# Optimization experiments

Measured on AMD Instinct MI355X. Metric: run time of the kernel, lower is better.

Reference implementation:

```python
import jax, jax.numpy as jnp
import numpy as np

N, C, E, B, NPG, MAX_LEN, H, EF = 16384, 512, 524288, 64, 256, 512, 8, 16
EPS = 1e-5

def layernorm(x, g, b):
    m = jnp.mean(x, axis=-1, keepdims=True)
    v = jnp.mean(jnp.square(x - m), axis=-1, keepdims=True)
    return (x - m) / jnp.sqrt(v + EPS) * g + b

def setup_inputs() -> dict:
    key = jax.random.key(0)
    ks = list(jax.random.split(key, 32))
    x = jax.random.normal(ks[0], (N, C), dtype=jnp.float32)
    edge_attr = jax.random.normal(ks[1], (E, EF), dtype=jnp.float32)
    # edges within each graph of NPG nodes
    src = jax.random.randint(ks[2], (E,), 0, N)
    dst = (src // NPG) * NPG + jax.random.randint(ks[3], (E,), 0, NPG)
    edge_index = jnp.stack([src, dst]).astype(jnp.int64)
    batch = jnp.repeat(jnp.arange(B), NPG).astype(jnp.int64)  # sorted graph ids
    s = 0.03
    p = lambda k, shp: jax.random.normal(k, shp, dtype=jnp.float32) * s
    return dict(
        x=x, edge_attr=edge_attr,
        gcn_w=p(ks[4], (C, C)), gcn_b=jnp.zeros((C,)),
        ep_w=p(ks[5], (EF, C)), ep_b=jnp.zeros((C,)),
        gate_w=p(ks[6], (2 * C, C)), gate_b=jnp.zeros((C,)),
        n1_g=jnp.ones((C,)), n1_b=jnp.zeros((C,)),
        in_w=p(ks[7], (C, 3 * C)), in_b=jnp.zeros((3 * C,)),
        out_w=p(ks[8], (C, C)), out_b=jnp.zeros((C,)),
        tn_g=jnp.ones((C,)), tn_b=jnp.zeros((C,)),
        m_w1=p(ks[9], (C, 2 * C)), m_b1=jnp.zeros((2 * C,)),
        m_w2=p(ks[10], (2 * C, C)), m_b2=jnp.zeros((C,)),
        fn_g=jnp.ones((C,)), fn_b=jnp.zeros((C,)),
        edge_index=edge_index, batch=batch,
    )

def reference(x, edge_attr, gcn_w, gcn_b, ep_w, ep_b, gate_w, gate_b,
              n1_g, n1_b, in_w, in_b, out_w, out_b, tn_g, tn_b,
              m_w1, m_b1, m_w2, m_b2, fn_g, fn_b, edge_index, batch):
    src, dst = edge_index[0], edge_index[1]
    # --- CoGNN: weighted GCN conv (self-loops, sym norm) ---
    ew = jax.lax.stop_gradient(jnp.sqrt(jnp.sum(edge_attr * edge_attr, axis=-1)))
    loop = jnp.arange(N)
    src2 = jnp.concatenate([src, loop]); dst2 = jnp.concatenate([dst, loop])
    ew2 = jnp.concatenate([ew, jnp.ones((N,), ew.dtype)])
    deg = jax.ops.segment_sum(ew2, dst2, num_segments=N)
    dinv = jnp.where(deg > 0, jax.lax.rsqrt(jnp.maximum(deg, 1e-12)), 0.0)
    norm = dinv[src2] * ew2 * dinv[dst2]
    xw = x @ gcn_w
    x_conv = jax.ops.segment_sum(norm[:, None] * xw[src2], dst2, num_segments=N) + gcn_b
    # edge_proj -> scatter_add at source nodes (dropout = identity in eval)
    ef = jax.nn.relu(edge_attr @ ep_w + ep_b)
    ef = jax.ops.segment_sum(ef, src, num_segments=N)
    gate = jax.nn.sigmoid(jnp.concatenate([x_conv, ef], axis=-1) @ gate_w + gate_b)
    x1 = gate * x_conv + (1.0 - gate) * ef
    x1 = jax.nn.relu(layernorm(x1, n1_g, n1_b))
    x = x1 + x  # identity residual (in_channels == hidden_channels)
    # --- to_dense_batch ---
    counts = jax.ops.segment_sum(jnp.ones((N,), jnp.int32), batch, num_segments=B)
    starts = jnp.cumsum(counts) - counts
    pos = jnp.arange(N) - starts[batch]
    xd = jnp.zeros((B, MAX_LEN, C), x.dtype).at[batch, pos].set(x)
    maskd = jnp.zeros((B, MAX_LEN), bool).at[batch, pos].set(True)
    # --- MHA (batch_first, key_padding_mask = ~mask) ---
    Dh = C // H
    qkv = xd @ in_w + in_b
    q, k, v = jnp.split(qkv, 3, axis=-1)
    q = q.reshape(B, MAX_LEN, H, Dh); k = k.reshape(B, MAX_LEN, H, Dh); v = v.reshape(B, MAX_LEN, H, Dh)
    scores = jnp.einsum('blhd,bmhd->bhlm', q, k) / jnp.sqrt(jnp.asarray(Dh, x.dtype))
    scores = jnp.where(maskd[:, None, None, :], scores, -1e9)
    attn = jax.nn.softmax(scores, axis=-1)
    o = jnp.einsum('bhlm,bmhd->blhd', attn, v).reshape(B, MAX_LEN, C)
    o = o @ out_w + out_b
    x_global = o[batch, pos]  # undo dense batching: x_global[mask]
    x = layernorm(x + x_global, tn_g, tn_b)
    # --- MLP ---
    x = x + (jax.nn.silu(x @ m_w1 + m_b1) @ m_w2 + m_b2)
    return layernorm(x, fn_g, fn_b)
```

## Files before the change

### kernel.cpp

```cpp
#include <hip/hip_runtime.h>

#define NN 16384
#define CC 512
#define EE 524288
#define BB 64
#define HH 8
#define EFD 16
#define GEMAXE 10240

typedef __bf16 bf16_t;
typedef __bf16 bf16x4 __attribute__((ext_vector_type(4)));
typedef __bf16 bf16x8 __attribute__((ext_vector_type(8)));
typedef float f32x4v __attribute__((ext_vector_type(4)));

__device__ __forceinline__ float2 ldb2(const bf16_t* p) {
  unsigned w = *(const unsigned*)p;
  return make_float2(__uint_as_float(w << 16), __uint_as_float(w & 0xFFFF0000u));
}

__device__ __forceinline__ int2 xcd_swizzle() {
  int nwg = gridDim.x * gridDim.y;
  int bid = blockIdx.y * gridDim.x + blockIdx.x;
  int wg = (bid & 7) * (nwg >> 3) + (bid >> 3);
  return make_int2(wg % gridDim.x, wg / gridDim.x);
}


__global__ void init_kernel(int* ghist, int* nid_src, bf16_t* eacsr) {
  int i = threadIdx.x;
  if (i < 64) ghist[i] = 0;
  if (i < 32) nid_src[EE + i] = -1;
  ((int*)(eacsr + (size_t)EE * 16))[i] = 0;
}

__global__ __launch_bounds__(256) void edge_pass1(const int* __restrict__ dst,
                                                  int* ghist) {
  __shared__ int h[64];
  int tid = threadIdx.x;
  if (tid < 64) h[tid] = 0;
  __syncthreads();
  int e = blockIdx.x * 256 + tid;
  atomicAdd(&h[dst[e] >> 8], 1);
  __syncthreads();
  if (tid < 64 && h[tid]) atomicAdd(&ghist[tid], h[tid]);
}

__global__ void gexscan_kernel(const int* __restrict__ ghist, int* __restrict__ gstart,
                               int* __restrict__ gcur) {
  if (threadIdx.x == 0) {
    int s = 0;
    for (int g = 0; g < 64; ++g) { gstart[g] = s; gcur[g] = s; s += ghist[g]; }
    gstart[64] = s;
  }
}

__global__ __launch_bounds__(256) void graph_scatter_kernel(
    const int* __restrict__ src, const int* __restrict__ dst,
    const float* __restrict__ ea, int* gcur, int2* __restrict__ grec,
    float* __restrict__ ewg) {
  __shared__ int h[64], base[64], h2[64];
  int tid = threadIdx.x;
  if (tid < 64) { h[tid] = 0; h2[tid] = 0; }
  __syncthreads();
  int e0 = blockIdx.x * 2048;
  int gloc[8];
#pragma unroll
  for (int k = 0; k < 8; ++k) {
    gloc[k] = dst[e0 + k * 256 + tid] >> 8;
    atomicAdd(&h[gloc[k]], 1);
  }
  __syncthreads();
  if (tid < 64) base[tid] = h[tid] ? atomicAdd(&gcur[tid], h[tid]) : 0;
  __syncthreads();
#pragma unroll
  for (int k = 0; k < 8; ++k) {
    int e = e0 + k * 256 + tid;
    int g = gloc[k];
    int p = atomicAdd(&h2[g], 1);
    int pos = base[g] + p;
    int ls = src[e] & 255;
    int ld = dst[e] & 255;
    grec[pos] = make_int2(e | (ls << 19), ld);
    const float4* pa = (const float4*)(ea + (size_t)e * EFD);
    float s = 0.f;
#pragma unroll
    for (int q = 0; q < 4; ++q) {
      float4 v = pa[q];
      s += v.x * v.x + v.y * v.y + v.z * v.z + v.w * v.w;
    }
    ewg[pos] = sqrtf(s);
  }
}

__global__ __launch_bounds__(1024) void graph_sort2_kernel(
    const int2* __restrict__ grec, const float* __restrict__ ewg,
    const int* __restrict__ gstart, int* __restrict__ elist_src,
    int* __restrict__ nid_src, int* __restrict__ start_src,
    float2* __restrict__ dstrec, int* __restrict__ start_dst,
    float* __restrict__ dinv) {
  __shared__ int lbuf[GEMAXE];
  __shared__ unsigned short sl[GEMAXE];
  __shared__ float ewl[GEMAXE];
  __shared__ int h[256], hx[256], h2[256];
  __shared__ float fdinv[256];
  const int g = blockIdx.x & 63;
  const int tid = threadIdx.x;
  const int gs = gstart[g];
  const int cnt = gstart[g + 1] - gs;
  if (tid < 256) { h[tid] = 0; h2[tid] = 0; }
  __syncthreads();
  if (blockIdx.x < 64) {
    for (int i = tid; i < cnt; i += 1024) {
      int2 r = grec[gs + i];
      int ld = r.y;
      sl[i] = (unsigned short)(((r.x >> 19) & 255) | (ld << 8));
      ewl[i] = ewg[gs + i];
      atomicAdd(&h[ld], 1);
    }
    __syncthreads();
    int myc = (tid < 256) ? h[tid] : 0;
    for (int off = 1; off < 256; off <<= 1) {
      int v = (tid < 256 && tid >= off) ? h[tid - off] : 0;
      __syncthreads();
      if (tid < 256) h[tid] += v;
      __syncthreads();
    }
    if (tid < 256) {
      hx[tid] = h[tid] - myc;
      start_dst[g * 256 + tid] = gs + hx[tid];
    }
    if (g == 63 && tid == 0) start_dst[NN] = EE;
    __syncthreads();
    for (int i = tid; i < cnt; i += 1024) {
      int ld = sl[i] >> 8;
      int p = hx[ld] + atomicAdd(&h2[ld], 1);
      lbuf[p] = i;
    }
    __syncthreads();
    if (tid < 256) {
      float dg = 1.0f;
      int s0 = hx[tid], e0 = s0 + myc;
      for (int i = s0; i < e0; ++i) dg += ewl[lbuf[i]];
      float dv = rsqrtf(fmaxf(dg, 1e-12f));
      fdinv[tid] = dv;
      dinv[g * 256 + tid] = dv;
    }
    __syncthreads();
    for (int p = tid; p < cnt; p += 1024) {
      int i = lbuf[p];
      int ls = sl[i] & 255;
      int ld = sl[i] >> 8;
      dstrec[gs + p] =
          make_float2(fdinv[ls] * ewl[i] * fdinv[ld], __int_as_float(ls));
    }
  } else {
    int* wb = (int*)ewl;
    for (int i = tid; i < cnt; i += 1024) {
      int w = grec[gs + i].x;
      wb[i] = w;
      atomicAdd(&h[w >> 19], 1);
    }
    __syncthreads();
    int myc = (tid < 256) ? h[tid] : 0;
    for (int off = 1; off < 256; off <<= 1) {
      int v = (tid < 256 && tid >= off) ? h[tid - off] : 0;
      __syncthreads();
      if (tid < 256) h[tid] += v;
      __syncthreads();
    }
    if (tid < 256) {
      hx[tid] = h[tid] - myc;
      start_src[g * 256 + tid] = gs + hx[tid];
    }
    if (g == 63 && tid == 0) start_src[NN] = EE;
    __syncthreads();
    for (int i = tid; i < cnt; i += 1024) {
      int w = wb[i];
      int ls = w >> 19;
      int p = hx[ls] + atomicAdd(&h2[ls], 1);
      lbuf[p] = w;
    }
    __syncthreads();
    for (int p = tid; p < cnt; p += 1024) {
      int w = lbuf[p];
      elist_src[gs + p] = w & 0x7FFFF;
      nid_src[gs + p] = g * 256 + (w >> 19);
    }
  }
}

__global__ void ea_gather_kernel(const float* __restrict__ ea,
                                 const int* __restrict__ elist,
                                 bf16_t* __restrict__ eacsr) {
  int idx = blockIdx.x * 256 + threadIdx.x;
  if (idx >= EE * 2) return;
  int pos = idx >> 1, half = idx & 1;
  int e = elist[pos];
  const f32x4v* p = (const f32x4v*)(ea + (size_t)e * EFD + half * 8);
  f32x4v u0 = p[0], u1 = p[1];
  bf16x8 f;
#pragma unroll
  for (int r = 0; r < 4; ++r) {
    f[r] = (bf16_t)u0[r];
    f[4 + r] = (bf16_t)u1[r];
  }
  *(bf16x8*)(eacsr + (size_t)pos * 16 + half * 8) = f;
}

__global__ __launch_bounds__(256) void an_build_kernel(
    const float2* __restrict__ dstrec, const int* __restrict__ start_dst,
    const float* __restrict__ dinv, bf16_t* __restrict__ An) {
  __shared__ float AnS[128][256];
  const int g = blockIdx.x >> 1, h = blockIdx.x & 1;
  const int tid = threadIdx.x;
  float4* az = (float4*)&AnS[0][0];
  for (int i = tid; i < 128 * 256 / 4; i += 256)
    az[i] = make_float4(0.f, 0.f, 0.f, 0.f);
  __syncthreads();
  const int nbase = g * 256 + h * 128;
  if (tid < 128) {
    int node = nbase + tid;
    int st = start_dst[node], en = start_dst[node + 1];
    float* row = AnS[tid];
    for (int p = st; p < en; ++p) {
      float2 r = dstrec[p];
      row[__float_as_int(r.y)] += r.x;
    }
    float dv = dinv[node];
    row[h * 128 + tid] += dv * dv;
  }
  __syncthreads();
  bf16_t* out = An + (size_t)nbase * 256;
  const float* s0 = &AnS[0][0];
  for (int i = tid; i < 128 * 256 / 8; i += 256) {
    bf16x8 v;
#pragma unroll
    for (int r = 0; r < 8; ++r) v[r] = (bf16_t)s0[i * 8 + r];
    *(bf16x8*)(out + i * 8) = v;
  }
}


__global__ void cvt_bf16_kernel(const float* __restrict__ in, bf16_t* __restrict__ out,
                                int n4) {
  int i = blockIdx.x * 256 + threadIdx.x;
  if (i >= n4) return;
  float4 v = ((const float4*)in)[i];
  bf16x4 o;
  o[0] = (bf16_t)v.x; o[1] = (bf16_t)v.y; o[2] = (bf16_t)v.z; o[3] = (bf16_t)v.w;
  ((bf16x4*)out)[i] = o;
}

__global__ __launch_bounds__(256) void wt_kernel(const float* __restrict__ W,
                                                 bf16_t* __restrict__ Wt, int K, int N) {
  __shared__ float tile[32][33];
  int bx = blockIdx.x * 32;
  int by = blockIdx.y * 32;
  int tx = threadIdx.x & 31, ty = threadIdx.x >> 5;
#pragma unroll
  for (int i = 0; i < 32; i += 8)
    tile[ty + i][tx] = W[(size_t)(by + ty + i) * N + bx + tx];
  __syncthreads();
#pragma unroll
  for (int i = 0; i < 32; i += 8)
    Wt[(size_t)(bx + ty + i) * K + by + tx] = (bf16_t)tile[tx][ty + i];
}

__global__ __launch_bounds__(512) void ef_mfma_kernel(
    const bf16_t* __restrict__ eacsr, const float* __restrict__ ep_w,
    const float* __restrict__ ep_b, const int* __restrict__ nid,
    const int* __restrict__ start, bf16_t* __restrict__ efb) {
  const int tid = threadIdx.x;
  const int lane = tid & 63;
  const int wv = tid >> 6;
  const int l15 = lane & 15;
  const int g = lane >> 4;
  const int n0 = blockIdx.x * 16;
  const int cbase = wv * 64;

  bf16x8 wfr[4];
#pragma unroll
  for (int t = 0; t < 4; ++t) {
    bf16x8 f = {};
    int c = cbase + t * 16 + l15;
    if (g < 2) {
#pragma unroll
      for (int j = 0; j < 8; ++j) f[j] = (bf16_t)ep_w[(g * 8 + j) * CC + c];
    } else if (g == 2) {
      f[0] = (bf16_t)ep_b[c];
    }
    wfr[t] = f;
  }

  const int st = start[n0];
  const int en = start[n0 + 16];
  const int tgt = n0 + l15;

  f32x4v eacc[4] = {};

  for (int cb = st; cb < en; cb += 32) {
    bf16x8 af[2];
#pragma unroll
    for (int mE = 0; mE < 2; ++mE) {
      bf16x8 f = {};
      if (g < 2) {
        f = *(const bf16x8*)(eacsr + (size_t)(cb + mE * 16 + l15) * 16 + g * 8);
      } else if (g == 2) {
        f[0] = (bf16_t)1.0f;
      }
      af[mE] = f;
    }
    int4 idlo = *(const int4*)(nid + cb + g * 4);
    int4 idhi = *(const int4*)(nid + cb + 16 + g * 4);
    bf16x8 sf;
    sf[0] = (idlo.x == tgt) ? (bf16_t)1.0f : (bf16_t)0.0f;
    sf[1] = (idlo.y == tgt) ? (bf16_t)1.0f : (bf16_t)0.0f;
    sf[2] = (idlo.z == tgt) ? (bf16_t)1.0f : (bf16_t)0.0f;
    sf[3] = (idlo.w == tgt) ? (bf16_t)1.0f : (bf16_t)0.0f;
    sf[4] = (idhi.x == tgt) ? (bf16_t)1.0f : (bf16_t)0.0f;
    sf[5] = (idhi.y == tgt) ? (bf16_t)1.0f : (bf16_t)0.0f;
    sf[6] = (idhi.z == tgt) ? (bf16_t)1.0f : (bf16_t)0.0f;
    sf[7] = (idhi.w == tgt) ? (bf16_t)1.0f : (bf16_t)0.0f;
#pragma unroll
    for (int t = 0; t < 4; ++t) {
      f32x4v s0 = {}, s1 = {};
      s0 = __builtin_amdgcn_mfma_f32_16x16x32_bf16(af[0], wfr[t], s0, 0, 0, 0);
      s1 = __builtin_amdgcn_mfma_f32_16x16x32_bf16(af[1], wfr[t], s1, 0, 0, 0);
      union { bf16x8 v; bf16x4 h[2]; } pf;
#pragma unroll
      for (int r = 0; r < 4; ++r) {
        pf.h[0][r] = (bf16_t)fmaxf(s0[r], 0.f);
        pf.h[1][r] = (bf16_t)fmaxf(s1[r], 0.f);
      }
      eacc[t] = __builtin_amdgcn_mfma_f32_16x16x32_bf16(sf, pf.v, eacc[t], 0, 0, 0);
    }
  }
#pragma unroll
  for (int t = 0; t < 4; ++t) {
    int c = cbase + t * 16 + l15;
#pragma unroll
    for (int r = 0; r < 4; ++r) {
      int node = n0 + g * 4 + r;
      efb[(size_t)node * (2 * CC) + CC + c] = (bf16_t)eacc[t][r];
    }
  }
}

__device__ __forceinline__ void gl_lds16(const bf16_t* g, bf16_t* l) {
  __builtin_amdgcn_global_load_lds(
      (const __attribute__((address_space(1))) void*)g,
      (__attribute__((address_space(3))) void*)l, 16, 0, 0);
}

template <int ACT, int OUT>
__global__ __launch_bounds__(256) void gemm_bf16_kernel(
    const bf16_t* __restrict__ A, const bf16_t* __restrict__ Bt,
    const float* __restrict__ bias, void* __restrict__ Cout, int M, int N, int K) {
  __shared__ __align__(16) bf16_t Al[128 * 64];
  __shared__ __align__(16) bf16_t Bl[128 * 64];
  const int tid = threadIdx.x;
  const int lane = tid & 63;
  const int wave = tid >> 6;
  int2 sw = xcd_swizzle();
  const int row0 = sw.y * 128;
  const int col0 = sw.x * 128;
  const int wm = (wave >> 1) * 64;
  const int wn = (wave & 1) * 64;
  f32x4v acc[4][4] = {};
  const int srow = wave * 8 + (lane >> 3);
  const int sslot = (lane & 7) ^ (lane >> 3);
  const bf16_t* aBase = A + (size_t)(row0 + srow) * K + sslot * 8;
  const bf16_t* bBase = Bt + (size_t)(col0 + srow) * K + sslot * 8;
  const int fr = lane & 15;
  const int g = lane >> 4;
  const int f7 = fr & 7;
  for (int k0 = 0; k0 < K; k0 += 64) {
#pragma unroll
    for (int i = 0; i < 4; ++i)
      gl_lds16(aBase + (size_t)(i * 32) * K + k0, Al + i * 2048 + wave * 512);
#pragma unroll
    for (int i = 0; i < 4; ++i)
      gl_lds16(bBase + (size_t)(i * 32) * K + k0, Bl + i * 2048 + wave * 512);
    __syncthreads();
#pragma unroll
    for (int s = 0; s < 2; ++s) {
      const int sl = ((s * 4 + g) ^ f7) * 8;
      bf16x8 af[4], bfv[4];
#pragma unroll
      for (int m = 0; m < 4; ++m)
        af[m] = *(const bf16x8*)(Al + (wm + m * 16 + fr) * 64 + sl);
#pragma unroll
      for (int n = 0; n < 4; ++n)
        bfv[n] = *(const bf16x8*)(Bl + (wn + n * 16 + fr) * 64 + sl);
#pragma unroll
      for (int m = 0; m < 4; ++m)
#pragma unroll
        for (int n = 0; n < 4; ++n)
          acc[m][n] = __builtin_amdgcn_mfma_f32_16x16x32_bf16(af[m], bfv[n],
                                                              acc[m][n], 0, 0, 0);
    }
    __syncthreads();
  }
  const int fq = (lane >> 4) * 4;
#pragma unroll
  for (int m = 0; m < 4; ++m) {
    int grb = row0 + wm + m * 16 + fq;
#pragma unroll
    for (int n = 0; n < 4; ++n) {
      int gc = col0 + wn + n * 16 + fr;
      float bv = bias ? bias[gc] : 0.f;
#pragma unroll
      for (int r = 0; r < 4; ++r) {
        float v = acc[m][n][r] + bv;
        if (ACT == 1) v = v / (1.f + __expf(-v));
        if (OUT == 0)
          ((float*)Cout)[(size_t)(grb + r) * N + gc] = v;
        else
          ((bf16_t*)Cout)[(size_t)(grb + r) * N + gc] = (bf16_t)v;
      }
    }
  }
}

__global__ __launch_bounds__(256) void an_gemm_kernel(
    const bf16_t* __restrict__ An, const bf16_t* __restrict__ xwT,
    const float* __restrict__ bias, bf16_t* __restrict__ outb) {
  __shared__ __align__(16) bf16_t Al[128 * 64];
  __shared__ __align__(16) bf16_t Bl[128 * 64];
  const int tid = threadIdx.x;
  const int lane = tid & 63;
  const int wave = tid >> 6;
  int2 sw = xcd_swizzle();
  const int row0 = sw.y * 128;
  const int col0 = sw.x * 128;
  const int gr = row0 >> 8;
  f32x4v acc[4][4] = {};
  const int srow = wave * 8 + (lane >> 3);
  const int sslot = (lane & 7) ^ (lane >> 3);
  const bf16_t* aBase = An + (size_t)(row0 + srow) * 256 + sslot * 8;
  const bf16_t* bBase = xwT + (size_t)(col0 + srow) * NN + gr * 256 + sslot * 8;
  const int wm = (wave >> 1) * 64;
  const int wn = (wave & 1) * 64;
  const int fr = lane & 15;
  const int g = lane >> 4;
  const int f7 = fr & 7;
  for (int k0 = 0; k0 < 256; k0 += 64) {
#pragma unroll
    for (int i = 0; i < 4; ++i)
      gl_lds16(aBase + (size_t)(i * 32) * 256 + k0, Al + i * 2048 + wave * 512);
#pragma unroll
    for (int i = 0; i < 4; ++i)
      gl_lds16(bBase + (size_t)(i * 32) * NN + k0, Bl + i * 2048 + wave * 512);
    __syncthreads();
#pragma unroll
    for (int s = 0; s < 2; ++s) {
      const int sl = ((s * 4 + g) ^ f7) * 8;
      bf16x8 af[4], bfv[4];
#pragma unroll
      for (int m = 0; m < 4; ++m)
        af[m] = *(const bf16x8*)(Al + (wm + m * 16 + fr) * 64 + sl);
#pragma unroll
      for (int n = 0; n < 4; ++n)
        bfv[n] = *(const bf16x8*)(Bl + (wn + n * 16 + fr) * 64 + sl);
#pragma unroll
      for (int m = 0; m < 4; ++m)
#pragma unroll
        for (int n = 0; n < 4; ++n)
          acc[m][n] = __builtin_amdgcn_mfma_f32_16x16x32_bf16(af[m], bfv[n],
                                                              acc[m][n], 0, 0, 0);
    }
    __syncthreads();
  }
  const int fq = (lane >> 4) * 4;
#pragma unroll
  for (int m = 0; m < 4; ++m) {
    int grb = row0 + wm + m * 16 + fq;
#pragma unroll
    for (int n = 0; n < 4; ++n) {
      int gc = col0 + wn + n * 16 + fr;
      float bv = bias[gc];
#pragma unroll
      for (int r = 0; r < 4; ++r)
        outb[(size_t)(grb + r) * (2 * CC) + gc] = (bf16_t)(acc[m][n][r] + bv);
    }
  }
}


__device__ inline void block_reduce2(float& s, float& q, float* red) {
#pragma unroll
  for (int off = 32; off >= 1; off >>= 1) {
    s += __shfl_xor(s, off, 64);
    q += __shfl_xor(q, off, 64);
  }
  int wid = threadIdx.x >> 6;
  if ((threadIdx.x & 63) == 0) { red[wid * 2] = s; red[wid * 2 + 1] = q; }
  __syncthreads();
  s = red[0] + red[2] + red[4] + red[6];
  q = red[1] + red[3] + red[5] + red[7];
}

template <int IA, int IB, int WF>
__global__ __launch_bounds__(256) void ln_addT_kernel(
    const void* __restrict__ A, const void* __restrict__ Bv,
    const float* __restrict__ g, const float* __restrict__ be,
    float* __restrict__ outf, bf16_t* __restrict__ outb) {
  int row = blockIdx.x, tid = threadIdx.x, c0 = tid * 2;
  __shared__ float red[8];
  float2 a = IA ? ldb2((const bf16_t*)A + (size_t)row * CC + c0)
                : *(const float2*)((const float*)A + (size_t)row * CC + c0);
  float2 b = IB ? ldb2((const bf16_t*)Bv + (size_t)row * CC + c0)
                : *(const float2*)((const float*)Bv + (size_t)row * CC + c0);
  float x0 = a.x + b.x, x1 = a.y + b.y;
  float s = x0 + x1, q = x0 * x0 + x1 * x1;
  block_reduce2(s, q, red);
  float mean = s * (1.f / CC);
  float var = q * (1.f / CC) - mean * mean;
  float rs = rsqrtf(var + 1e-5f);
  float o0 = (x0 - mean) * rs * g[c0] + be[c0];
  float o1 = (x1 - mean) * rs * g[c0 + 1] + be[c0 + 1];
  if (WF) {
    *(float2*)(outf + (size_t)row * CC + c0) = make_float2(o0, o1);
  } else {
    outb[(size_t)row * CC + c0] = (bf16_t)o0;
    outb[(size_t)row * CC + c0 + 1] = (bf16_t)o1;
  }
}

__global__ __launch_bounds__(256) void ln_gate_kernel(
    const bf16_t* __restrict__ gpreb, const float* __restrict__ gate_b,
    const bf16_t* __restrict__ xcef, const float* __restrict__ n1g,
    const float* __restrict__ n1b, const float* __restrict__ xin,
    bf16_t* __restrict__ x2b) {
  int row = blockIdx.x, tid = threadIdx.x, c0 = tid * 2;
  __shared__ float red[8];
  float2 gp = ldb2(gpreb + (size_t)row * CC + c0);
  float2 xcv = ldb2(xcef + (size_t)row * (2 * CC) + c0);
  float2 efv = ldb2(xcef + (size_t)row * (2 * CC) + CC + c0);
  float g0 = 1.f / (1.f + __expf(-(gp.x + gate_b[c0])));
  float g1 = 1.f / (1.f + __expf(-(gp.y + gate_b[c0 + 1])));
  float x0 = g0 * xcv.x + (1.f - g0) * efv.x;
  float x1 = g1 * xcv.y + (1.f - g1) * efv.y;
  float s = x0 + x1, q = x0 * x0 + x1 * x1;
  block_reduce2(s, q, red);
  float mean = s * (1.f / CC);
  float var = q * (1.f / CC) - mean * mean;
  float rs = rsqrtf(var + 1e-5f);
  float2 xi = *(const float2*)(xin + (size_t)row * CC + c0);
  float o0 = fmaxf((x0 - mean) * rs * n1g[c0] + n1b[c0], 0.f) + xi.x;
  float o1 = fmaxf((x1 - mean) * rs * n1g[c0 + 1] + n1b[c0 + 1], 0.f) + xi.y;
  x2b[(size_t)row * CC + c0] = (bf16_t)o0;
  x2b[(size_t)row * CC + c0 + 1] = (bf16_t)o1;
}

__global__ __launch_bounds__(256) void vt_pack_kernel(const bf16_t* __restrict__ qkvb,
                                                      bf16_t* __restrict__ vt) {
  int b = blockIdx.x >> 3, h = blockIdx.x & 7;
  int nb = b * 256;
  size_t voff = 1024 + (size_t)h * 64;
  char* out = (char*)(vt + (size_t)blockIdx.x * (64 * 256));
  __shared__ bf16_t tile[64][80];
  int tid = threadIdx.x;
  for (int kb = 0; kb < 4; ++kb) {
    __syncthreads();
#pragma unroll
    for (int p = 0; p < 2; ++p) {
      int k = p * 32 + (tid >> 3);
      int d8 = tid & 7;
      bf16x8 v = *(const bf16x8*)(qkvb + (size_t)(nb + kb * 64 + k) * 1536 + voff + d8 * 8);
      *(bf16x8*)(&tile[k][d8 * 8]) = v;
    }
    __syncthreads();
#pragma unroll
    for (int p = 0; p < 2; ++p) {
      int d = p * 32 + (tid >> 3);
      int k8 = tid & 7;
      bf16x8 v;
#pragma unroll
      for (int j = 0; j < 8; ++j) {
        int pos = k8 * 8 + j;
        int sl = pos & 31;
        int srck = (pos & 32) + ((sl >> 3) << 2) + (sl & 3) + (((sl >> 2) & 1) << 4);
        v[j] = tile[srck][d];
      }
      int byteoff = d * 512 + ((kb * 128 + k8 * 16) ^ ((d & 7) << 4));
      *(bf16x8*)(out + byteoff) = v;
    }
  }
}

__global__ __launch_bounds__(256, 2) void attn_mfma_kernel(
    const bf16_t* __restrict__ qkvb, const bf16_t* __restrict__ vt,
    bf16_t* __restrict__ o) {
  const int b = blockIdx.x >> 3;
  const int h = blockIdx.x & 7;
  const int nb = b * 256;
  const int tid = threadIdx.x;
  const int lane = tid & 63;
  const int wv = tid >> 6;
  const int l15 = lane & 15;
  const int g = lane >> 4;
  const int swzk = (l15 & 7) << 4;
  __shared__ __align__(16) bf16_t Klds[256 * 64];
  __shared__ __align__(16) bf16_t Vtlds[64 * 256];
  const size_t qoff = (size_t)h * 64;
  const size_t koff = 512 + (size_t)h * 64;

  {
    const int dcol = 16 * ((tid & 7) ^ ((tid >> 3) & 7));
    const bf16_t* srcb = qkvb + koff + (dcol >> 1);
#pragma unroll
    for (int i = 0; i < 8; ++i) {
      int k = i * 32 + (tid >> 3);
      gl_lds16(srcb + (size_t)(nb + k) * 1536, Klds + ((i * 4096 + wv * 1024) >> 1));
    }
  }
  {
    const bf16_t* vsrc = vt + (size_t)blockIdx.x * (64 * 256);
#pragma unroll
    for (int i = 0; i < 8; ++i) {
      int base = i * 4096 + wv * 1024;
      gl_lds16(vsrc + ((base >> 1) + lane * 8), Vtlds + (base >> 1));
    }
  }

  bf16x8 qf[4][2];
#pragma unroll
  for (int n = 0; n < 4; ++n) {
    const bf16_t* qp = qkvb + (size_t)(nb + wv * 64 + 16 * n + l15) * 1536 + qoff + g * 8;
    qf[n][0] = *(const bf16x8*)(qp);
    qf[n][1] = *(const bf16x8*)(qp + 32);
  }

  __syncthreads();

  f32x4v oacc[4][4] = {};
  float mrun[4] = {-1e30f, -1e30f, -1e30f, -1e30f};
  float lrun[4] = {0.f, 0.f, 0.f, 0.f};

  for (int kc = 0; kc < 4; ++kc) {
    f32x4v sacc[4][4] = {};
    const int kb128 = (kc * 64 + l15) * 128;
#pragma unroll
    for (int m = 0; m < 4; ++m) {
      bf16x8 a0 = *(const bf16x8*)(Klds + ((kb128 + m * 2048 + ((g * 16) ^ swzk)) >> 1));
      bf16x8 a1 =
          *(const bf16x8*)(Klds + ((kb128 + m * 2048 + ((64 + g * 16) ^ swzk)) >> 1));
#pragma unroll
      for (int n = 0; n < 4; ++n) {
        sacc[m][n] = __builtin_amdgcn_mfma_f32_16x16x32_bf16(a0, qf[n][0], sacc[m][n], 0, 0, 0);
        sacc[m][n] = __builtin_amdgcn_mfma_f32_16x16x32_bf16(a1, qf[n][1], sacc[m][n], 0, 0, 0);
      }
    }
    uint2 pb[4][4];
#pragma unroll
    for (int n = 0; n < 4; ++n) {
      float mx = sacc[0][n][0];
#pragma unroll
      for (int m = 0; m < 4; ++m)
#pragma unroll
        for (int r = 0; r < 4; ++r) mx = fmaxf(mx, sacc[m][n][r]);
      mx = fmaxf(mx, __shfl_xor(mx, 16));
      mx = fmaxf(mx, __shfl_xor(mx, 32));
      float mnew = fmaxf(mrun[n], mx);
      float c = __expf((mrun[n] - mnew) * 0.125f);
      mrun[n] = mnew;
      float s = 0.f;
#pragma unroll
      for (int m = 0; m < 4; ++m) {
        float p0 = __expf((sacc[m][n][0] - mnew) * 0.125f);
        float p1 = __expf((sacc[m][n][1] - mnew) * 0.125f);
        float p2 = __expf((sacc[m][n][2] - mnew) * 0.125f);
        float p3 = __expf((sacc[m][n][3] - mnew) * 0.125f);
        s += (p0 + p1) + (p2 + p3);
        union { bf16x4 v; uint2 u; } cv;
        cv.v[0] = (bf16_t)p0; cv.v[1] = (bf16_t)p1;
        cv.v[2] = (bf16_t)p2; cv.v[3] = (bf16_t)p3;
        pb[m][n] = cv.u;
      }
      s += __shfl_xor(s, 16);
      s += __shfl_xor(s, 32);
      lrun[n] = lrun[n] * c + s;
#pragma unroll
      for (int m = 0; m < 4; ++m)
#pragma unroll
        for (int r = 0; r < 4; ++r) oacc[m][n][r] *= c;
    }
#pragma unroll
    for (int h2 = 0; h2 < 2; ++h2) {
      bf16x8 vf[4];
#pragma unroll
      for (int m = 0; m < 4; ++m)
        vf[m] = *(const bf16x8*)(Vtlds + (((16 * m + l15) * 512 +
                                          ((kc * 128 + h2 * 64 + g * 16) ^ swzk)) >> 1));
#pragma unroll
      for (int n = 0; n < 4; ++n) {
        union { uint2 u[2]; bf16x8 v; } pf;
        pf.u[0] = pb[2 * h2][n];
        pf.u[1] = pb[2 * h2 + 1][n];
#pragma unroll
        for (int m = 0; m < 4; ++m)
          oacc[m][n] =
              __builtin_amdgcn_mfma_f32_16x16x32_bf16(vf[m], pf.v, oacc[m][n], 0, 0, 0);
      }
    }
  }
  float inv[4];
#pragma unroll
  for (int n = 0; n < 4; ++n) inv[n] = 1.0f / lrun[n];
#pragma unroll
  for (int m = 0; m < 4; ++m)
#pragma unroll
    for (int n = 0; n < 4; ++n) {
      bf16x4 pk;
#pragma unroll
      for (int r = 0; r < 4; ++r) pk[r] = (bf16_t)(oacc[m][n][r] * inv[n]);
      *(bf16x4*)(o + (size_t)(nb + wv * 64 + 16 * n + l15) * 512 + h * 64 + 16 * m +
                 4 * g) = pk;
    }
}


static inline char* alignp(char* p, size_t a) {
  return (char*)(((uintptr_t)p + a - 1) & ~(uintptr_t)(a - 1));
}

extern "C" void kernel_launch(void* const* d_in, const int* in_sizes, int n_in,
                              void* d_out, int out_size, void* d_ws, size_t ws_size,
                              hipStream_t stream) {
  const float* x = (const float*)d_in[0];
  const float* edge_attr = (const float*)d_in[1];
  const float* gcn_w = (const float*)d_in[2];
  const float* gcn_b = (const float*)d_in[3];
  const float* ep_w = (const float*)d_in[4];
  const float* ep_b = (const float*)d_in[5];
  const float* gate_w = (const float*)d_in[6];
  const float* gate_b = (const float*)d_in[7];
  const float* n1_g = (const float*)d_in[8];
  const float* n1_b = (const float*)d_in[9];
  const float* in_w = (const float*)d_in[10];
  const float* in_b = (const float*)d_in[11];
  const float* out_w = (const float*)d_in[12];
  const float* out_b = (const float*)d_in[13];
  const float* tn_g = (const float*)d_in[14];
  const float* tn_b = (const float*)d_in[15];
  const float* m_w1 = (const float*)d_in[16];
  const float* m_b1 = (const float*)d_in[17];
  const float* m_w2 = (const float*)d_in[18];
  const float* m_b2 = (const float*)d_in[19];
  const float* fn_g = (const float*)d_in[20];
  const float* fn_b = (const float*)d_in[21];
  const int* eidx = (const int*)d_in[22];
  const int* src = eidx;
  const int* dst = eidx + EE;

  float* ws = (float*)d_ws;
  float* R1 = ws;
  float* R2 = R1 + (size_t)NN * 3 * CC;
  float* R3 = R2 + (size_t)NN * CC;
  float* R4 = R3 + (size_t)NN * CC;
  float* dinv = R4 + (size_t)NN * CC;
  int* ip = (int*)(dinv + NN);
  int* ghist = ip;      ip += 64;
  int* gstart = ip;     ip += 65;
  int* gcur = ip;       ip += 64;
  int* elist_src = ip;  ip += EE;
  int* nid_src = ip;    ip += EE + 32;
  int* start_src = ip;  ip += NN + 1;
  int* start_dst = ip;  ip += NN + 1;
  char* bp = alignp((char*)ip, 64);
  int2* grec = (int2*)bp;             bp += (size_t)EE * 8;
  float* ewg = (float*)bp;            bp += (size_t)EE * 4;
  float2* dstrec = (float2*)bp;       bp += (size_t)EE * 8;
  bf16_t* x2b = (bf16_t*)bp;          bp += (size_t)NN * CC * 2;
  bf16_t* gcn_wt = (bf16_t*)bp;       bp += (size_t)CC * CC * 2;
  bf16_t* gate_wt = (bf16_t*)bp;      bp += (size_t)CC * 2 * CC * 2;
  bf16_t* in_wt = (bf16_t*)bp;        bp += (size_t)3 * CC * CC * 2;
  bf16_t* out_wt = (bf16_t*)bp;       bp += (size_t)CC * CC * 2;
  bf16_t* m_w1t = (bf16_t*)bp;        bp += (size_t)2 * CC * CC * 2;
  bf16_t* m_w2t = (bf16_t*)bp;        bp += (size_t)CC * 2 * CC * 2;

  bf16_t* xb = (bf16_t*)R1;
  bf16_t* xcefb = (bf16_t*)R1;
  bf16_t* qkvb = (bf16_t*)R1;
  bf16_t* hb = (bf16_t*)R1;
  bf16_t* eacsr = (bf16_t*)((char*)R1 + (size_t)64 * 1024 * 1024);
  bf16_t* xwT = (bf16_t*)R2;
  bf16_t* gpreb = (bf16_t*)R2;
  bf16_t* ob = (bf16_t*)R2;
  bf16_t* vt = ob + (size_t)NN * CC;
  bf16_t* x3b = (bf16_t*)R2;
  bf16_t* AnFull = (bf16_t*)R3;
  bf16_t* oprjb = (bf16_t*)R4;
  float* yf = R4;

  init_kernel<<<1, 256, 0, stream>>>(ghist, nid_src, eacsr);
  edge_pass1<<<EE / 256, 256, 0, stream>>>(dst, ghist);
  gexscan_kernel<<<1, 64, 0, stream>>>(ghist, gstart, gcur);
  graph_scatter_kernel<<<EE / 2048, 256, 0, stream>>>(src, dst, edge_attr, gcur,
                                                      grec, ewg);
  graph_sort2_kernel<<<128, 1024, 0, stream>>>(grec, ewg, gstart, elist_src, nid_src,
                                               start_src, dstrec, start_dst, dinv);
  ea_gather_kernel<<<(EE * 2 + 255) / 256, 256, 0, stream>>>(edge_attr, elist_src,
                                                             eacsr);
  an_build_kernel<<<128, 256, 0, stream>>>(dstrec, start_dst, dinv, AnFull);

  wt_kernel<<<dim3(CC / 32, CC / 32), 256, 0, stream>>>(gcn_w, gcn_wt, CC, CC);
  wt_kernel<<<dim3(CC / 32, 2 * CC / 32), 256, 0, stream>>>(gate_w, gate_wt, 2 * CC, CC);
  wt_kernel<<<dim3(3 * CC / 32, CC / 32), 256, 0, stream>>>(in_w, in_wt, CC, 3 * CC);
  wt_kernel<<<dim3(CC / 32, CC / 32), 256, 0, stream>>>(out_w, out_wt, CC, CC);
  wt_kernel<<<dim3(2 * CC / 32, CC / 32), 256, 0, stream>>>(m_w1, m_w1t, CC, 2 * CC);
  wt_kernel<<<dim3(CC / 32, 2 * CC / 32), 256, 0, stream>>>(m_w2, m_w2t, 2 * CC, CC);

  cvt_bf16_kernel<<<(NN * CC / 4 + 255) / 256, 256, 0, stream>>>(x, xb, NN * CC / 4);
  gemm_bf16_kernel<0, 1><<<dim3(NN / 128, CC / 128), 256, 0, stream>>>(
      gcn_wt, xb, nullptr, xwT, CC, NN, CC);
  an_gemm_kernel<<<dim3(CC / 128, NN / 128), 256, 0, stream>>>(AnFull, xwT, gcn_b,
                                                               xcefb);
  ef_mfma_kernel<<<NN / 16, 512, 0, stream>>>(eacsr, ep_w, ep_b, nid_src, start_src,
                                              xcefb);
  dim3 gA(CC / 128, NN / 128);
  gemm_bf16_kernel<0, 1><<<gA, 256, 0, stream>>>(xcefb, gate_wt, nullptr, gpreb, NN,
                                                 CC, 2 * CC);
  ln_gate_kernel<<<NN, 256, 0, stream>>>(gpreb, gate_b, xcefb, n1_g, n1_b, x, x2b);

  dim3 gQ(3 * CC / 128, NN / 128);
  gemm_bf16_kernel<0, 1><<<gQ, 256, 0, stream>>>(x2b, in_wt, in_b, qkvb, NN, 3 * CC, CC);
  vt_pack_kernel<<<BB * HH, 256, 0, stream>>>(qkvb, vt);
  attn_mfma_kernel<<<BB * HH, 256, 0, stream>>>(qkvb, vt, ob);
  gemm_bf16_kernel<0, 1><<<gA, 256, 0, stream>>>(ob, out_wt, out_b, oprjb, NN, CC, CC);
  ln_addT_kernel<1, 1, 0><<<NN, 256, 0, stream>>>(x2b, oprjb, tn_g, tn_b, nullptr, x3b);

  dim3 gH(2 * CC / 128, NN / 128);
  gemm_bf16_kernel<1, 1><<<gH, 256, 0, stream>>>(x3b, m_w1t, m_b1, hb, NN, 2 * CC, CC);
  gemm_bf16_kernel<0, 0><<<gA, 256, 0, stream>>>(hb, m_w2t, m_b2, yf, NN, CC, 2 * CC);
  ln_addT_kernel<1, 0, 1><<<NN, 256, 0, stream>>>(x3b, yf, fn_g, fn_b, (float*)d_out,
                                                  nullptr);
}
```

Baseline: 442.9 us.

## Double-buffer GEMM LDS tiles with BK=32 to overlap loads and MFMA

```diff
diff --git a/kernel.cpp b/kernel.cpp
--- a/kernel.cpp
+++ b/kernel.cpp
@@ -356,8 +356,8 @@
 __global__ __launch_bounds__(256) void gemm_bf16_kernel(
     const bf16_t* __restrict__ A, const bf16_t* __restrict__ Bt,
     const float* __restrict__ bias, void* __restrict__ Cout, int M, int N, int K) {
-  __shared__ __align__(16) bf16_t Al[128 * 64];
-  __shared__ __align__(16) bf16_t Bl[128 * 64];
+  __shared__ __align__(16) bf16_t Al[2][128 * 32];
+  __shared__ __align__(16) bf16_t Bl[2][128 * 32];
   const int tid = threadIdx.x;
   const int lane = tid & 63;
   const int wave = tid >> 6;
@@ -367,38 +367,43 @@
   const int wm = (wave >> 1) * 64;
   const int wn = (wave & 1) * 64;
   f32x4v acc[4][4] = {};
-  const int srow = wave * 8 + (lane >> 3);
-  const int sslot = (lane & 7) ^ (lane >> 3);
-  const bf16_t* aBase = A + (size_t)(row0 + srow) * K + sslot * 8;
-  const bf16_t* bBase = Bt + (size_t)(col0 + srow) * K + sslot * 8;
+  const int srow = tid >> 2;
+  const int sslot8 = (((tid & 3) ^ (srow & 3))) * 8;
+  const bf16_t* aBase = A + (size_t)(row0 + srow) * K + sslot8;
+  const bf16_t* bBase = Bt + (size_t)(col0 + srow) * K + sslot8;
+  const int ldsOff = wave * 512;
   const int fr = lane & 15;
   const int g = lane >> 4;
-  const int f7 = fr & 7;
-  for (int k0 = 0; k0 < K; k0 += 64) {
-#pragma unroll
-    for (int i = 0; i < 4; ++i)
-      gl_lds16(aBase + (size_t)(i * 32) * K + k0, Al + i * 2048 + wave * 512);
-#pragma unroll
-    for (int i = 0; i < 4; ++i)
-      gl_lds16(bBase + (size_t)(i * 32) * K + k0, Bl + i * 2048 + wave * 512);
-    __syncthreads();
-#pragma unroll
-    for (int s = 0; s < 2; ++s) {
-      const int sl = ((s * 4 + g) ^ f7) * 8;
-      bf16x8 af[4], bfv[4];
-#pragma unroll
-      for (int m = 0; m < 4; ++m)
-        af[m] = *(const bf16x8*)(Al + (wm + m * 16 + fr) * 64 + sl);
+  const int f3 = fr & 3;
+  const int nt = K >> 5;
+  gl_lds16(aBase, Al[0] + ldsOff);
+  gl_lds16(aBase + (size_t)64 * K, Al[0] + 2048 + ldsOff);
+  gl_lds16(bBase, Bl[0] + ldsOff);
+  gl_lds16(bBase + (size_t)64 * K, Bl[0] + 2048 + ldsOff);
+  __syncthreads();
+  for (int t = 0; t < nt; ++t) {
+    int cur = t & 1;
+    if (t + 1 < nt) {
+      int k0 = (t + 1) << 5;
+      gl_lds16(aBase + k0, Al[cur ^ 1] + ldsOff);
+      gl_lds16(aBase + (size_t)64 * K + k0, Al[cur ^ 1] + 2048 + ldsOff);
+      gl_lds16(bBase + k0, Bl[cur ^ 1] + ldsOff);
+      gl_lds16(bBase + (size_t)64 * K + k0, Bl[cur ^ 1] + 2048 + ldsOff);
+    }
+    const int sl = (g ^ f3) * 8;
+    bf16x8 af[4], bfv[4];
+#pragma unroll
+    for (int m = 0; m < 4; ++m)
+      af[m] = *(const bf16x8*)(Al[cur] + (wm + m * 16 + fr) * 32 + sl);
+#pragma unroll
+    for (int n = 0; n < 4; ++n)
+      bfv[n] = *(const bf16x8*)(Bl[cur] + (wn + n * 16 + fr) * 32 + sl);
+#pragma unroll
+    for (int m = 0; m < 4; ++m)
 #pragma unroll
       for (int n = 0; n < 4; ++n)
-        bfv[n] = *(const bf16x8*)(Bl + (wn + n * 16 + fr) * 64 + sl);
-#pragma unroll
-      for (int m = 0; m < 4; ++m)
-#pragma unroll
-        for (int n = 0; n < 4; ++n)
-          acc[m][n] = __builtin_amdgcn_mfma_f32_16x16x32_bf16(af[m], bfv[n],
-                                                              acc[m][n], 0, 0, 0);
-    }
+        acc[m][n] =
+            __builtin_amdgcn_mfma_f32_16x16x32_bf16(af[m], bfv[n], acc[m][n], 0, 0, 0);
     __syncthreads();
   }
   const int fq = (lane >> 4) * 4;
```

Result: no change. 448.1 us (+1.2%).
